# Kernel optimization log

Measured on AMD Instinct MI355X. Metric: run time of the kernel, lower is better.

## Reference

```python
import jax, jax.numpy as jnp
import numpy as np

LOC_SIZE, CID_SIZE, UID_SIZE, TIM_SIZE = 10000, 300, 1000, 48
LOC_EMB, CID_EMB, UID_EMB, TIM_EMB = 256, 64, 64, 32
HID, ENC_HID = 500, 250            # hidden_size, history_hidden_size
SEQ, TGT = 2048, 256
INPUT = LOC_EMB + TIM_EMB + CID_EMB  # 352


def setup_inputs() -> dict:
    key = jax.random.key(0)
    ks = jax.random.split(key, 32)
    n = lambda i, shape, s=0.05: (jax.random.normal(ks[i], shape, dtype=jnp.float32) * s)
    d = {}
    d["loc"] = jax.random.randint(ks[0], (SEQ, 1), 0, LOC_SIZE)
    d["tim"] = jax.random.randint(ks[1], (SEQ, 1), 0, TIM_SIZE)
    d["cid"] = jax.random.randint(ks[2], (SEQ, 1), 0, CID_SIZE)
    d["uid"] = jax.random.randint(ks[3], (1,), 0, UID_SIZE)
    d["target"] = jax.random.randint(ks[4], (TGT, 1), 0, LOC_SIZE)
    d["target_len"] = TGT
    d["time_sim_matrix"] = jax.random.uniform(ks[5], (TIM_SIZE, TIM_SIZE), dtype=jnp.float32)
    # keep distances away from 0 since the model computes 1/dist
    d["poi_distance_matrix"] = jax.random.uniform(ks[6], (LOC_SIZE, LOC_SIZE), dtype=jnp.float32, minval=0.1, maxval=2.0)
    d["poi_cid_tim"] = jax.random.uniform(ks[7], (TIM_SIZE, CID_SIZE), dtype=jnp.float32)
    # embedding tables (emb_loc/emb_cid are pretrained+frozen in the original)
    d["weight"] = n(8, (LOC_SIZE, LOC_EMB))
    d["weight_cid"] = n(9, (CID_SIZE, CID_EMB))
    d["emb_uid_w"] = n(10, (UID_SIZE, UID_EMB))
    d["emb_tim_w"] = n(11, (TIM_SIZE, TIM_EMB))
    # bidirectional encoder LSTM (hidden 250), gate order i,f,g,o like torch
    d["enc_Wih_f"] = n(12, (4 * ENC_HID, INPUT))
    d["enc_Whh_f"] = n(13, (4 * ENC_HID, ENC_HID))
    d["enc_b_f"] = jnp.zeros((4 * ENC_HID,), jnp.float32)
    d["enc_Wih_b"] = n(14, (4 * ENC_HID, INPUT))
    d["enc_Whh_b"] = n(15, (4 * ENC_HID, ENC_HID))
    d["enc_b_b"] = jnp.zeros((4 * ENC_HID,), jnp.float32)
    # decoder LSTM (hidden 500)
    d["dec_Wih"] = n(16, (4 * HID, INPUT))
    d["dec_Whh"] = n(17, (4 * HID, HID))
    d["dec_b"] = jnp.zeros((4 * HID,), jnp.float32)
    # linear layers
    d["fc_user_w"] = n(18, (HID, UID_EMB))
    d["fc_user_b"] = jnp.zeros((HID,), jnp.float32)
    d["fc_final_w"] = n(19, (LOC_SIZE, 3 * HID))
    d["fc_final_b"] = jnp.zeros((LOC_SIZE,), jnp.float32)
    d["fc_final2_w"] = n(20, (HID, 3 * HID))
    d["fc_final2_b"] = jnp.zeros((HID,), jnp.float32)
    return d


def _lstm(x, Wih, Whh, b, H):
    """Single-layer LSTM, batch=1. x: [T, D] -> hs: [T, H]."""
    h0 = jnp.zeros((H,), x.dtype)
    c0 = jnp.zeros((H,), x.dtype)

    def step(carry, xt):
        h, c = carry
        z = Wih @ xt + Whh @ h + b
        i, f, g, o = jnp.split(z, 4)
        c = jax.nn.sigmoid(f) * c + jax.nn.sigmoid(i) * jnp.tanh(g)
        h = jax.nn.sigmoid(o) * jnp.tanh(c)
        return (h, c), h

    _, hs = jax.lax.scan(step, (h0, c0), x)
    return hs


def _table_attn(history, current, table, invert=False, causal=False):
    """Vectorized replacement for the nested-loop lookup attention.
    energies[i, j] = table[current[i], history[j]] (or its reciprocal),
    upper triangle left at 0 for the self-attn variants (as in the original),
    then softmax over the full row (torch F.softmax default dim=1 on 2D)."""
    e = table[current[:, None], history[None, :]]
    if invert:
        e = 1.0 / e
    if causal:
        nn_ = e.shape[0]
        e = jnp.where(jnp.tril(jnp.ones((nn_, nn_), bool)), e, jnp.zeros((), e.dtype))
    return jax.nn.softmax(e, axis=-1)


def reference(loc, tim, cid, uid, target, target_len,
              time_sim_matrix, poi_distance_matrix, poi_cid_tim,
              weight, weight_cid, emb_uid_w, emb_tim_w,
              enc_Wih_f, enc_Whh_f, enc_b_f, enc_Wih_b, enc_Whh_b, enc_b_b,
              dec_Wih, dec_Whh, dec_b,
              fc_user_w, fc_user_b, fc_final_w, fc_final_b, fc_final2_w, fc_final2_b):
    T = int(target_len)
    loc_f, tim_f, cid_f = loc[:, 0], tim[:, 0], cid[:, 0]

    # cross attention: current window attends to history via lookup tables
    attn_cid_time = _table_attn(cid_f[:-T], tim_f[-T:], poi_cid_tim)
    attn_loc = _table_attn(loc_f[:-T], loc_f[-T:], poi_distance_matrix, invert=True)
    attn_time = _table_attn(tim_f[:-T], tim_f[-T:], time_sim_matrix)
    # self attention on the current window (lower-triangular fill)
    self_cid_time = _table_attn(cid_f[-T:], tim_f[-T:], poi_cid_tim, causal=True)
    self_loc = _table_attn(loc_f[-T:], loc_f[-T:], poi_distance_matrix, invert=True, causal=True)
    self_time = _table_attn(tim_f[-T:], tim_f[-T:], time_sim_matrix, causal=True)

    # embeddings (dropout is identity in eval)
    x = jnp.concatenate([weight[loc_f], emb_tim_w[tim_f], weight_cid[cid_f]], axis=1)  # [SEQ, INPUT]
    hist_x, tgt_x = x[:-T], x[-T:]

    # bidirectional encoder over history
    hf = _lstm(hist_x, enc_Wih_f, enc_Whh_f, enc_b_f, ENC_HID)
    hb = _lstm(hist_x[::-1], enc_Wih_b, enc_Whh_b, enc_b_b, ENC_HID)[::-1]
    hidden_history = jnp.concatenate([hf, hb], axis=1)  # [SEQ-T, 2*ENC_HID=500]

    # decoder over current window
    hidden_state = _lstm(tgt_x, dec_Wih, dec_Whh, dec_b, HID)  # [T, 500]

    target_emb = weight[target[:, 0]]  # [T, LOC_EMB]

    uid_emb = emb_uid_w[uid] @ fc_user_w.T + fc_user_b  # [1, 500]
    user_attn = jax.nn.softmax(uid_emb @ hidden_history.T, axis=-1)  # [1, hist]
    context_user = user_attn @ hidden_history  # [1, 500]

    context = (attn_loc + attn_time + attn_cid_time) @ hidden_history  # [T, 500]
    hidden_state = (self_loc + self_time + self_cid_time) @ hidden_state  # [T, 500]

    hidden_state_all = hidden_state + uid_emb  # broadcast of repeat
    out = jnp.concatenate([hidden_state_all, context,
                           jnp.broadcast_to(context_user, (T, HID))], axis=1)  # [T, 1500]
    y = out @ fc_final_w.T + fc_final_b    # [T, LOC_SIZE]
    y1 = out @ fc_final2_w.T + fc_final2_b  # [T, HID]
    score = jax.nn.log_softmax(y, axis=-1)
    return score, y1, target_emb
```

## Files before the change

kernel.cpp:

```cpp
#include <hip/hip_runtime.h>
#include <stdint.h>

#define HIST 1792
#define TGT 256
#define SEQ 2048
#define INPUT 352
#define EHID 250
#define HID 500

typedef _Float16 h2_t __attribute__((ext_vector_type(2)));

static __device__ __forceinline__ float fdot2(uint32_t a, uint32_t b, float c) {
  return __builtin_amdgcn_fdot2(__builtin_bit_cast(h2_t, a),
                                __builtin_bit_cast(h2_t, b), c, false);
}
static __device__ __forceinline__ uint32_t packh2(float lo, float hi) {
  h2_t h; h[0] = (_Float16)lo; h[1] = (_Float16)hi;
  return __builtin_bit_cast(uint32_t, h);
}
static __device__ __forceinline__ uint4 packq(const float* p) {
  uint4 r;
  r.x = packh2(p[0], p[1]); r.y = packh2(p[2], p[3]);
  r.z = packh2(p[4], p[5]); r.w = packh2(p[6], p[7]);
  return r;
}
static __device__ __forceinline__ float dotq(uint4 w, uint4 h, float acc) {
  acc = fdot2(w.x, h.x, acc); acc = fdot2(w.y, h.y, acc);
  acc = fdot2(w.z, h.z, acc); acc = fdot2(w.w, h.w, acc);
  return acc;
}
static __device__ __forceinline__ float sigf(float x) {
  x = fminf(fmaxf(x, -30.f), 30.f);
  return 1.f / (1.f + __expf(-x));
}
static __device__ __forceinline__ float tanh_f(float x) {
  x = fminf(fmaxf(x, -15.f), 15.f);
  float e = __expf(2.f * x);
  return (e - 1.f) / (e + 1.f);
}
static __device__ __forceinline__ void spin_flag(volatile int* f) {
  while (__hip_atomic_load(f, __ATOMIC_ACQUIRE, __HIP_MEMORY_SCOPE_AGENT) == 0)
    __builtin_amdgcn_s_sleep(2);
}
#define AW(dst, src) asm("v_accvgpr_write_b32 %0, %1" : "=a"(dst) : "v"(src))
#define AR(dst, src) asm("v_accvgpr_read_b32 %0, %1" : "=v"(dst) : "a"(src))
#define ARQ(dst, arr, base) do { AR(dst.x, arr[(base)+0]); AR(dst.y, arr[(base)+1]); AR(dst.z, arr[(base)+2]); AR(dst.w, arr[(base)+3]); } while(0)

__global__ void k_embed(const int* __restrict__ loc, const int* __restrict__ tim,
                        const int* __restrict__ cid, const int* __restrict__ target,
                        const float* __restrict__ weight, const float* __restrict__ emb_tim_w,
                        const float* __restrict__ weight_cid,
                        float* __restrict__ x, float* __restrict__ te) {
  int t = blockIdx.x, tid = threadIdx.x;
  if (t < SEQ) {
    int l = loc[t], tm = tim[t], cd = cid[t];
    float* xr = x + (size_t)t * INPUT;
    for (int k = tid; k < 256; k += blockDim.x) xr[k] = weight[(size_t)l * 256 + k];
    for (int k = tid; k < 32; k += blockDim.x)  xr[256 + k] = emb_tim_w[tm * 32 + k];
    for (int k = tid; k < 64; k += blockDim.x)  xr[288 + k] = weight_cid[cd * 64 + k];
  } else {
    int i = t - SEQ;
    int tg = target[i];
    for (int k = tid; k < 256; k += blockDim.x) te[(size_t)i * 256 + k] = weight[(size_t)tg * 256 + k];
  }
}

__global__ void k_gemm_t16(const float* __restrict__ A, int lda,
                           const float* __restrict__ W, const float* __restrict__ bias,
                           float* __restrict__ C, int ldc,
                           int M, int N, int K, int revA) {
  __shared__ uint32_t AsP[8][65];
  __shared__ uint32_t WsP[8][65];
  const int bn = blockIdx.x * 64, bm = blockIdx.y * 64;
  const int tid = threadIdx.x;
  const int tx = tid & 15, ty = tid >> 4;
  float acc[4][4] = {};
  for (int k0 = 0; k0 < K; k0 += 16) {
    for (int i = tid; i < 512; i += 256) {
      int m = i & 63, kk = i >> 6;
      int gm = bm + m, gk = k0 + 2 * kk;
      float v0 = 0.f, v1 = 0.f;
      if (gm < M) {
        int am = revA ? (M - 1 - gm) : gm;
        if (gk < K)     v0 = A[(size_t)am * lda + gk];
        if (gk + 1 < K) v1 = A[(size_t)am * lda + gk + 1];
      }
      AsP[kk][m] = packh2(v0, v1);
    }
    for (int i = tid; i < 512; i += 256) {
      int n = i & 63, kk = i >> 6;
      int gn = bn + n, gk = k0 + 2 * kk;
      float v0 = 0.f, v1 = 0.f;
      if (gn < N) {
        if (gk < K)     v0 = W[(size_t)gn * K + gk];
        if (gk + 1 < K) v1 = W[(size_t)gn * K + gk + 1];
      }
      WsP[kk][n] = packh2(v0, v1);
    }
    __syncthreads();
#pragma unroll
    for (int kk = 0; kk < 8; kk++) {
      uint32_t a0 = AsP[kk][ty * 4 + 0], a1 = AsP[kk][ty * 4 + 1], a2 = AsP[kk][ty * 4 + 2], a3 = AsP[kk][ty * 4 + 3];
      uint32_t b0 = WsP[kk][tx * 4 + 0], b1 = WsP[kk][tx * 4 + 1], b2 = WsP[kk][tx * 4 + 2], b3 = WsP[kk][tx * 4 + 3];
      acc[0][0] = fdot2(a0, b0, acc[0][0]); acc[0][1] = fdot2(a0, b1, acc[0][1]);
      acc[0][2] = fdot2(a0, b2, acc[0][2]); acc[0][3] = fdot2(a0, b3, acc[0][3]);
      acc[1][0] = fdot2(a1, b0, acc[1][0]); acc[1][1] = fdot2(a1, b1, acc[1][1]);
      acc[1][2] = fdot2(a1, b2, acc[1][2]); acc[1][3] = fdot2(a1, b3, acc[1][3]);
      acc[2][0] = fdot2(a2, b0, acc[2][0]); acc[2][1] = fdot2(a2, b1, acc[2][1]);
      acc[2][2] = fdot2(a2, b2, acc[2][2]); acc[2][3] = fdot2(a2, b3, acc[2][3]);
      acc[3][0] = fdot2(a3, b0, acc[3][0]); acc[3][1] = fdot2(a3, b1, acc[3][1]);
      acc[3][2] = fdot2(a3, b2, acc[3][2]); acc[3][3] = fdot2(a3, b3, acc[3][3]);
    }
    __syncthreads();
  }
  for (int i = 0; i < 4; i++) {
    int gm = bm + ty * 4 + i; if (gm >= M) continue;
    for (int j = 0; j < 4; j++) {
      int gn = bn + tx * 4 + j; if (gn >= N) continue;
      C[(size_t)gm * ldc + gn] = acc[i][j] + (bias ? bias[gn] : 0.f);
    }
  }
}

__global__ void k_gemm_nn16(const float* __restrict__ A, int lda,
                            const float* __restrict__ B, int ldb,
                            const float* __restrict__ addvec,
                            float* __restrict__ C, int ldc,
                            int M, int N, int K) {
  __shared__ uint32_t AsP[8][65];
  __shared__ uint32_t BsP[8][65];
  const int bn = blockIdx.x * 64, bm = blockIdx.y * 64;
  const int tid = threadIdx.x;
  const int tx = tid & 15, ty = tid >> 4;
  float acc[4][4] = {};
  for (int k0 = 0; k0 < K; k0 += 16) {
    for (int i = tid; i < 512; i += 256) {
      int m = i & 63, kk = i >> 6;
      int gm = bm + m, gk = k0 + 2 * kk;
      float v0 = 0.f, v1 = 0.f;
      if (gm < M) {
        if (gk < K)     v0 = A[(size_t)gm * lda + gk];
        if (gk + 1 < K) v1 = A[(size_t)gm * lda + gk + 1];
      }
      AsP[kk][m] = packh2(v0, v1);
    }
    for (int i = tid; i < 512; i += 256) {
      int n = i & 63, kk = i >> 6;
      int gn = bn + n, gk = k0 + 2 * kk;
      float v0 = 0.f, v1 = 0.f;
      if (gn < N) {
        if (gk < K)     v0 = B[(size_t)gk * ldb + gn];
        if (gk + 1 < K) v1 = B[(size_t)(gk + 1) * ldb + gn];
      }
      BsP[kk][n] = packh2(v0, v1);
    }
    __syncthreads();
#pragma unroll
    for (int kk = 0; kk < 8; kk++) {
      uint32_t a0 = AsP[kk][ty * 4 + 0], a1 = AsP[kk][ty * 4 + 1], a2 = AsP[kk][ty * 4 + 2], a3 = AsP[kk][ty * 4 + 3];
      uint32_t b0 = BsP[kk][tx * 4 + 0], b1 = BsP[kk][tx * 4 + 1], b2 = BsP[kk][tx * 4 + 2], b3 = BsP[kk][tx * 4 + 3];
      acc[0][0] = fdot2(a0, b0, acc[0][0]); acc[0][1] = fdot2(a0, b1, acc[0][1]);
      acc[0][2] = fdot2(a0, b2, acc[0][2]); acc[0][3] = fdot2(a0, b3, acc[0][3]);
      acc[1][0] = fdot2(a1, b0, acc[1][0]); acc[1][1] = fdot2(a1, b1, acc[1][1]);
      acc[1][2] = fdot2(a1, b2, acc[1][2]); acc[1][3] = fdot2(a1, b3, acc[1][3]);
      acc[2][0] = fdot2(a2, b0, acc[2][0]); acc[2][1] = fdot2(a2, b1, acc[2][1]);
      acc[2][2] = fdot2(a2, b2, acc[2][2]); acc[2][3] = fdot2(a2, b3, acc[2][3]);
      acc[3][0] = fdot2(a3, b0, acc[3][0]); acc[3][1] = fdot2(a3, b1, acc[3][1]);
      acc[3][2] = fdot2(a3, b2, acc[3][2]); acc[3][3] = fdot2(a3, b3, acc[3][3]);
    }
    __syncthreads();
  }
  for (int i = 0; i < 4; i++) {
    int gm = bm + ty * 4 + i; if (gm >= M) continue;
    for (int j = 0; j < 4; j++) {
      int gn = bn + tx * 4 + j; if (gn >= N) continue;
      C[(size_t)gm * ldc + gn] = acc[i][j] + (addvec ? addvec[gn] : 0.f);
    }
  }
}

#define WQL 12
#define WBYTES (WQL * 512 * 16)
__launch_bounds__(512)
__global__ void k_lstm(const float* __restrict__ A_f, const float* __restrict__ A_b,
                       const float* __restrict__ A_d,
                       const float* __restrict__ Whh_f, const float* __restrict__ Whh_b,
                       const float* __restrict__ Whh_d,
                       float* __restrict__ hh, float* __restrict__ hdec,
                       float* zpub, uint32_t* hpub, int* flag_z, int* flag_h,
                       const int* __restrict__ loc, const int* __restrict__ tim,
                       const int* __restrict__ cid,
                       const float* __restrict__ ts, const float* __restrict__ pd,
                       const float* __restrict__ pct,
                       float* __restrict__ S1, float* __restrict__ S2,
                       const int* __restrict__ uid, const float* __restrict__ emb_uid_w,
                       const float* __restrict__ fc_user_w, const float* __restrict__ fc_user_b,
                       float* __restrict__ uid_emb) {
  const int b = blockIdx.x;
  const int tid = threadIdx.x;
  __shared__ __align__(16) unsigned char smem[WBYTES + 2048 + 4096];
  uint4* wl = (uint4*)smem;
  uint4* hbuf = (uint4*)(smem + WBYTES);
  float* zbuf = (float*)(smem + WBYTES + 2048);

  if (b < 6 && tid < 128) hbuf[tid] = make_uint4(0, 0, 0, 0);

  if (b < 2) {
    const float* A = (b == 0) ? A_f : A_b;
    const float* Whh = (b == 0) ? Whh_f : Whh_b;
    const bool act = tid < 500;
    uint4 wv0[10], wv1[10];
    uint32_t wa[128];
    if (act) {
      const float* wr0 = Whh + (size_t)tid * EHID;
      const float* wr1 = Whh + (size_t)(tid + 500) * EHID;
#pragma unroll
      for (int q = 0; q < 6; q++) {
        float t0[8], t1[8];
#pragma unroll
        for (int cc = 0; cc < 8; cc++) {
          int col = 208 + 8 * q + cc;
          t0[cc] = (col < EHID) ? wr0[col] : 0.f;
          t1[cc] = (col < EHID) ? wr1[col] : 0.f;
        }
        wl[(q * 2 + 0) * 512 + tid] = packq(t0);
        wl[(q * 2 + 1) * 512 + tid] = packq(t1);
      }
#pragma unroll
      for (int k = 0; k < 16; k++) {
        uint4 p0 = packq(wr0 + 8 * (10 + k));
        uint4 p1 = packq(wr1 + 8 * (10 + k));
        AW(wa[k * 4 + 0], p0.x); AW(wa[k * 4 + 1], p0.y);
        AW(wa[k * 4 + 2], p0.z); AW(wa[k * 4 + 3], p0.w);
        AW(wa[64 + k * 4 + 0], p1.x); AW(wa[64 + k * 4 + 1], p1.y);
        AW(wa[64 + k * 4 + 2], p1.z); AW(wa[64 + k * 4 + 3], p1.w);
      }
#pragma unroll
      for (int q = 0; q < 10; q++) { wv0[q] = packq(wr0 + 8 * q); wv1[q] = packq(wr1 + 8 * q); }
    }
    float c = 0.f;
    float aA = act ? A[tid] : 0.f;
    float aB = act ? A[500 + tid] : 0.f;
    __syncthreads();
    for (int t = 0; t < HIST; t++) {
      const uint4* hb = hbuf + (t & 1) * 32;
      if (act) {
        float z0 = aA, z1 = aB, y0 = 0.f, y1 = 0.f;
        int tn = (t + 1 < HIST) ? t + 1 : t;
        aA = A[tn * 1000 + tid];
        aB = A[tn * 1000 + 500 + tid];
#pragma unroll
        for (int q = 0; q < 10; q++) {
          uint4 hq = hb[q];
          z0 = dotq(wv0[q], hq, z0);
          z1 = dotq(wv1[q], hq, z1);
        }
#pragma unroll
        for (int k = 0; k < 16; k++) {
          uint4 hq = hb[10 + k];
          uint4 u0, u1;
          ARQ(u0, wa, k * 4);
          ARQ(u1, wa, 64 + k * 4);
          y0 = dotq(u0, hq, y0);
          y1 = dotq(u1, hq, y1);
        }
#pragma unroll
        for (int q = 0; q < 6; q++) {
          uint4 hq = hb[26 + q];
          z0 = dotq(wl[(q * 2 + 0) * 512 + tid], hq, z0);
          z1 = dotq(wl[(q * 2 + 1) * 512 + tid], hq, z1);
        }
        zbuf[tid] = z0 + y0;
        zbuf[500 + tid] = z1 + y1;
      }
      __syncthreads();
      float hval = 0.f;
      if (tid < EHID) {
        float zi = zbuf[tid], zf = zbuf[250 + tid], zg = zbuf[500 + tid], zo = zbuf[750 + tid];
        c = sigf(zf) * c + sigf(zi) * tanh_f(zg);
        hval = sigf(zo) * tanh_f(c);
        if (b == 0) hh[(size_t)t * HID + tid] = hval;
        else        hh[(size_t)(HIST - 1 - t) * HID + EHID + tid] = hval;
      }
      float hother = __shfl_xor(hval, 1);
      uint32_t* hw = (uint32_t*)(hbuf + ((t + 1) & 1) * 32);
      if (tid < EHID && !(tid & 1)) hw[tid >> 1] = packh2(hval, hother);
      __syncthreads();
    }
  } else if (b < 6) {
    const int gi = b - 2;
    const int j = tid;
    const bool act = (j < 500);
    uint4 wv[20];
    uint32_t wa[128];
    if (act) {
      const float* wr = Whh_d + (size_t)(gi * 500 + j) * HID;
#pragma unroll
      for (int q = 0; q < 12; q++) {
        float tmp[8];
#pragma unroll
        for (int cc = 0; cc < 8; cc++) {
          int col = 416 + 8 * q + cc;
          tmp[cc] = (col < HID) ? wr[col] : 0.f;
        }
        wl[q * 512 + tid] = packq(tmp);
      }
#pragma unroll
      for (int k = 0; k < 32; k++) {
        uint4 pq = packq(wr + 8 * (20 + k));
        AW(wa[k * 4 + 0], pq.x); AW(wa[k * 4 + 1], pq.y);
        AW(wa[k * 4 + 2], pq.z); AW(wa[k * 4 + 3], pq.w);
      }
#pragma unroll
      for (int q = 0; q < 20; q++) wv[q] = packq(wr + 8 * q);
    }
    float c = 0.f;
    float aD = act ? A_d[gi * 500 + j] : 0.f;
    __syncthreads();
    for (int t = 0; t < TGT; t++) {
      const uint4* hb = hbuf + (t & 1) * 64;
      float z = 0.f;
      if (act) {
        float z0 = aD, z1 = 0.f, z2 = 0.f, z3 = 0.f;
        int tn = (t + 1 < TGT) ? t + 1 : t;
        aD = A_d[tn * 2000 + gi * 500 + j];
#pragma unroll
        for (int q = 0; q < 20; q += 2) {
          z0 = dotq(wv[q], hb[q], z0);
          z1 = dotq(wv[q + 1], hb[q + 1], z1);
        }
#pragma unroll
        for (int k = 0; k < 32; k += 2) {
          uint4 u0, u1;
          ARQ(u0, wa, k * 4);
          ARQ(u1, wa, (k + 1) * 4);
          z2 = dotq(u0, hb[20 + k], z2);
          z3 = dotq(u1, hb[21 + k], z3);
        }
#pragma unroll
        for (int q = 0; q < 12; q += 2) {
          z0 = dotq(wl[q * 512 + tid], hb[52 + q], z0);
          z1 = dotq(wl[(q + 1) * 512 + tid], hb[53 + q], z1);
        }
        z = (z0 + z1) + (z2 + z3);
      }
      if (gi < 3) {
        if (act) zpub[gi * 512 + j] = z;
        __threadfence();
        __syncthreads();
        if (tid == 0) {
          __hip_atomic_store(&flag_z[t * 3 + gi], 1, __ATOMIC_RELEASE, __HIP_MEMORY_SCOPE_AGENT);
          spin_flag(&flag_h[t]);
        }
        __syncthreads();
        uint32_t* hw = (uint32_t*)(hbuf + ((t + 1) & 1) * 64);
        if (tid < 250)
          hw[tid] = __hip_atomic_load(&hpub[tid], __ATOMIC_RELAXED, __HIP_MEMORY_SCOPE_AGENT);
        __syncthreads();
      } else {
        if (tid == 0) {
          spin_flag(&flag_z[t * 3 + 0]);
          spin_flag(&flag_z[t * 3 + 1]);
          spin_flag(&flag_z[t * 3 + 2]);
        }
        __syncthreads();
        float hval = 0.f;
        if (act) {
          float zi = __hip_atomic_load(&zpub[0 * 512 + j], __ATOMIC_RELAXED, __HIP_MEMORY_SCOPE_AGENT);
          float zf = __hip_atomic_load(&zpub[1 * 512 + j], __ATOMIC_RELAXED, __HIP_MEMORY_SCOPE_AGENT);
          float zg = __hip_atomic_load(&zpub[2 * 512 + j], __ATOMIC_RELAXED, __HIP_MEMORY_SCOPE_AGENT);
          c = sigf(zf) * c + sigf(zi) * tanh_f(zg);
          hval = sigf(z) * tanh_f(c);
          hdec[(size_t)t * HID + j] = hval;
        }
        float hother = __shfl_xor(hval, 1);
        uint32_t* hw = (uint32_t*)(hbuf + ((t + 1) & 1) * 64);
        if (act && !(j & 1)) {
          uint32_t p = packh2(hval, hother);
          hw[j >> 1] = p;
          __hip_atomic_store(&hpub[j >> 1], p, __ATOMIC_RELAXED, __HIP_MEMORY_SCOPE_AGENT);
        }
        __threadfence();
        __syncthreads();
        if (tid == 0)
          __hip_atomic_store(&flag_h[t], 1, __ATOMIC_RELEASE, __HIP_MEMORY_SCOPE_AGENT);
      }
    }
  } else if (b < 262) {
    const int i = b - 6;
    float* e = (float*)smem;
    float* red = ((float*)smem) + HIST;
    const int loc_i = loc[HIST + i], tim_i = tim[HIST + i];
    for (int tab = 0; tab < 3; tab++) {
      for (int jj = tid; jj < HIST; jj += 512) {
        float v;
        if (tab == 0)      v = 1.f / pd[(size_t)loc_i * 10000 + loc[jj]];
        else if (tab == 1) v = ts[tim_i * 48 + tim[jj]];
        else               v = pct[tim_i * 300 + cid[jj]];
        e[jj] = v;
      }
      __syncthreads();
      float mx = -1e30f;
      for (int jj = tid; jj < HIST; jj += 512) mx = fmaxf(mx, e[jj]);
      red[tid] = mx; __syncthreads();
      for (int s = 256; s > 0; s >>= 1) { if (tid < s) red[tid] = fmaxf(red[tid], red[tid + s]); __syncthreads(); }
      mx = red[0]; __syncthreads();
      float sm = 0.f;
      for (int jj = tid; jj < HIST; jj += 512) sm += __expf(e[jj] - mx);
      red[tid] = sm; __syncthreads();
      for (int s = 256; s > 0; s >>= 1) { if (tid < s) red[tid] += red[tid + s]; __syncthreads(); }
      float inv = 1.f / red[0]; __syncthreads();
      for (int jj = tid; jj < HIST; jj += 512) {
        float p = __expf(e[jj] - mx) * inv;
        if (tab == 0) S1[(size_t)i * HIST + jj] = p; else S1[(size_t)i * HIST + jj] += p;
      }
      __syncthreads();
    }
    int lj = 0, tj = 0, cj = 0;
    if (tid < TGT) { lj = loc[HIST + tid]; tj = tim[HIST + tid]; cj = cid[HIST + tid]; }
    for (int tab = 0; tab < 3; tab++) {
      float v = 0.f;
      if (tid < TGT) {
        if (tab == 0)      v = 1.f / pd[(size_t)loc_i * 10000 + lj];
        else if (tab == 1) v = ts[tim_i * 48 + tj];
        else               v = pct[tim_i * 300 + cj];
        if (tid > i) v = 0.f;
        red[tid] = v;
      }
      __syncthreads();
      for (int s = 128; s > 0; s >>= 1) { if (tid < s) red[tid] = fmaxf(red[tid], red[tid + s]); __syncthreads(); }
      float mx = red[0]; __syncthreads();
      float ex = (tid < TGT) ? __expf(v - mx) : 0.f;
      if (tid < TGT) red[tid] = ex;
      __syncthreads();
      for (int s = 128; s > 0; s >>= 1) { if (tid < s) red[tid] += red[tid + s]; __syncthreads(); }
      float p = ex / red[0]; __syncthreads();
      if (tid < TGT) {
        if (tab == 0) S2[(size_t)i * TGT + tid] = p; else S2[(size_t)i * TGT + tid] += p;
      }
      __syncthreads();
    }
  } else {
    float* u = (float*)smem;
    if (tid < 64) u[tid] = emb_uid_w[(size_t)uid[0] * 64 + tid];
    __syncthreads();
    if (tid < HID) {
      float a = fc_user_b[tid];
      for (int k = 0; k < 64; k++) a += u[k] * fc_user_w[tid * 64 + k];
      uid_emb[tid] = a;
    }
  }
}

__global__ void k_user(const float* __restrict__ uid_emb, const float* __restrict__ hh,
                       float* __restrict__ out) {
  const int tid = threadIdx.x;
  __shared__ float s[HIST];
  __shared__ float red[1024];
  __shared__ __align__(16) float ue[HID];
  if (tid < HID) ue[tid] = uid_emb[tid];
  __syncthreads();
  for (int t = tid; t < HIST; t += 1024) {
    const float4* hr = (const float4*)(hh + (size_t)t * HID);
    const float4* uv = (const float4*)ue;
    float a = 0.f;
#pragma unroll 5
    for (int k = 0; k < 125; k++) {
      float4 h4 = hr[k], u4 = uv[k];
      a += h4.x * u4.x + h4.y * u4.y + h4.z * u4.z + h4.w * u4.w;
    }
    s[t] = a;
  }
  __syncthreads();
  float mx = -1e30f;
  for (int t = tid; t < HIST; t += 1024) mx = fmaxf(mx, s[t]);
  red[tid] = mx; __syncthreads();
  for (int st = 512; st > 0; st >>= 1) { if (tid < st) red[tid] = fmaxf(red[tid], red[tid + st]); __syncthreads(); }
  mx = red[0]; __syncthreads();
  float sm = 0.f;
  for (int t = tid; t < HIST; t += 1024) sm += __expf(s[t] - mx);
  red[tid] = sm; __syncthreads();
  for (int st = 512; st > 0; st >>= 1) { if (tid < st) red[tid] += red[tid + st]; __syncthreads(); }
  float inv = 1.f / red[0]; __syncthreads();
  for (int t = tid; t < HIST; t += 1024) s[t] = __expf(s[t] - mx) * inv;
  __syncthreads();
  if (tid < HID) {
    float a0 = 0.f, a1 = 0.f, a2 = 0.f, a3 = 0.f;
    for (int t = 0; t < HIST; t += 4) {
      a0 += s[t]     * hh[(size_t)t * HID + tid];
      a1 += s[t + 1] * hh[(size_t)(t + 1) * HID + tid];
      a2 += s[t + 2] * hh[(size_t)(t + 2) * HID + tid];
      a3 += s[t + 3] * hh[(size_t)(t + 3) * HID + tid];
    }
    float a = (a0 + a1) + (a2 + a3);
    for (int i = 0; i < TGT; i++) out[(size_t)i * 1500 + 1000 + tid] = a;
  }
}

__global__ void k_logsoftmax(float* __restrict__ y) {
  const int i = blockIdx.x;
  const int tid = threadIdx.x;
  float* r = y + (size_t)i * 10000;
  __shared__ float red[1024];
  float mx = -1e30f;
  for (int j = tid; j < 10000; j += 1024) mx = fmaxf(mx, r[j]);
  red[tid] = mx; __syncthreads();
  for (int s = 512; s > 0; s >>= 1) { if (tid < s) red[tid] = fmaxf(red[tid], red[tid + s]); __syncthreads(); }
  mx = red[0]; __syncthreads();
  float sm = 0.f;
  for (int j = tid; j < 10000; j += 1024) sm += __expf(r[j] - mx);
  red[tid] = sm; __syncthreads();
  for (int s = 512; s > 0; s >>= 1) { if (tid < s) red[tid] += red[tid + s]; __syncthreads(); }
  float lse = mx + __logf(red[0]);
  __syncthreads();
  for (int j = tid; j < 10000; j += 1024) r[j] = r[j] - lse;
}

extern "C" void kernel_launch(void* const* d_in, const int* in_sizes, int n_in,
                              void* d_out, int out_size, void* d_ws, size_t ws_size,
                              hipStream_t stream) {
  (void)in_sizes; (void)n_in; (void)out_size; (void)ws_size;
  const int* loc = (const int*)d_in[0];
  const int* tim = (const int*)d_in[1];
  const int* cid = (const int*)d_in[2];
  const int* uid = (const int*)d_in[3];
  const int* target = (const int*)d_in[4];
  const float* ts = (const float*)d_in[6];
  const float* pd = (const float*)d_in[7];
  const float* pct = (const float*)d_in[8];
  const float* weight = (const float*)d_in[9];
  const float* weight_cid = (const float*)d_in[10];
  const float* emb_uid_w = (const float*)d_in[11];
  const float* emb_tim_w = (const float*)d_in[12];
  const float* enc_Wih_f = (const float*)d_in[13];
  const float* enc_Whh_f = (const float*)d_in[14];
  const float* enc_b_f = (const float*)d_in[15];
  const float* enc_Wih_b = (const float*)d_in[16];
  const float* enc_Whh_b = (const float*)d_in[17];
  const float* enc_b_b = (const float*)d_in[18];
  const float* dec_Wih = (const float*)d_in[19];
  const float* dec_Whh = (const float*)d_in[20];
  const float* dec_b = (const float*)d_in[21];
  const float* fc_user_w = (const float*)d_in[22];
  const float* fc_user_b = (const float*)d_in[23];
  const float* fc_final_w = (const float*)d_in[24];
  const float* fc_final_b = (const float*)d_in[25];
  const float* fc_final2_w = (const float*)d_in[26];
  const float* fc_final2_b = (const float*)d_in[27];

  float* score = (float*)d_out;
  float* y1 = score + (size_t)TGT * 10000;
  float* te = y1 + (size_t)TGT * HID;

  float* ws = (float*)d_ws;
  float* x = ws;
  float* A_f = x + (size_t)SEQ * INPUT;
  float* A_b = A_f + (size_t)HIST * 1000;
  float* A_d = A_b + (size_t)HIST * 1000;
  float* hh = A_d + (size_t)TGT * 2000;
  float* hdec = hh + (size_t)HIST * HID;
  float* S1 = hdec + (size_t)TGT * HID;
  float* S2 = S1 + (size_t)TGT * HIST;
  float* outb = S2 + (size_t)TGT * TGT;
  float* uid_emb = outb + (size_t)TGT * 1500;
  float* zpub = uid_emb + 512;
  uint32_t* hpub = (uint32_t*)(zpub + 3 * 512);
  int* flag_z = (int*)(hpub + 256);
  int* flag_h = flag_z + 3 * TGT;

  k_embed<<<dim3(SEQ + TGT), dim3(128), 0, stream>>>(loc, tim, cid, target, weight, emb_tim_w, weight_cid, x, te);

  k_gemm_t16<<<dim3(16, 28), dim3(256), 0, stream>>>(x, INPUT, enc_Wih_f, enc_b_f, A_f, 1000, HIST, 1000, INPUT, 0);
  k_gemm_t16<<<dim3(16, 28), dim3(256), 0, stream>>>(x, INPUT, enc_Wih_b, enc_b_b, A_b, 1000, HIST, 1000, INPUT, 1);
  k_gemm_t16<<<dim3(32, 4), dim3(256), 0, stream>>>(x + (size_t)HIST * INPUT, INPUT, dec_Wih, dec_b, A_d, 2000, TGT, 2000, INPUT, 0);

  hipMemsetAsync(flag_z, 0, 4 * TGT * sizeof(int), stream);

  k_lstm<<<dim3(263), dim3(512), 0, stream>>>(A_f, A_b, A_d, enc_Whh_f, enc_Whh_b, dec_Whh,
                                              hh, hdec, zpub, hpub, flag_z, flag_h,
                                              loc, tim, cid, ts, pd, pct, S1, S2,
                                              uid, emb_uid_w, fc_user_w, fc_user_b, uid_emb);

  k_user<<<dim3(1), dim3(1024), 0, stream>>>(uid_emb, hh, outb);
  k_gemm_nn16<<<dim3(8, 4), dim3(256), 0, stream>>>(S2, TGT, hdec, HID, uid_emb, outb, 1500, TGT, HID, TGT);
  k_gemm_nn16<<<dim3(8, 4), dim3(256), 0, stream>>>(S1, HIST, hh, HID, nullptr, outb + 500, 1500, TGT, HID, HIST);

  k_gemm_t16<<<dim3(157, 4), dim3(256), 0, stream>>>(outb, 1500, fc_final_w, fc_final_b, score, 10000, TGT, 10000, 1500, 0);
  k_gemm_t16<<<dim3(8, 4), dim3(256), 0, stream>>>(outb, 1500, fc_final2_w, fc_final2_b, y1, 500, TGT, 500, 1500, 0);

  k_logsoftmax<<<dim3(TGT), dim3(1024), 0, stream>>>(score);
}
```

Measured before the change: 5.322 ms.

## Fuse input-projection GEMMs into LSTM kernel with chunk counters; fold user context into bias

Moves the encoder and decoder input-projection GEMMs into the persistent LSTM launch as extra blocks. Each block publishes completion through per-chunk atomic counters, and the recurrent blocks spin on those counters before consuming each 64-step chunk. This lets the recurrence start before all projections finish and removes separate launches. It also folds the constant context_user columns of the final linear layers into a precomputed bias, so the final GEMMs run with K=1000 instead of 1500. The risk is deadlock if the recurrent blocks are resident while the GEMM blocks cannot get scheduled, plus extra spin overhead.

```diff
diff --git a/kernel.cpp b/kernel.cpp
--- a/kernel.cpp
+++ b/kernel.cpp
@@ -40,6 +40,10 @@
 }
 static __device__ __forceinline__ void spin_flag(volatile int* f) {
   while (__hip_atomic_load(f, __ATOMIC_ACQUIRE, __HIP_MEMORY_SCOPE_AGENT) == 0)
+    __builtin_amdgcn_s_sleep(2);
+}
+static __device__ __forceinline__ void spin_cnt(volatile int* f, int target) {
+  while (__hip_atomic_load(f, __ATOMIC_ACQUIRE, __HIP_MEMORY_SCOPE_AGENT) < target)
     __builtin_amdgcn_s_sleep(2);
 }
 #define AW(dst, src) asm("v_accvgpr_write_b32 %0, %1" : "=a"(dst) : "v"(src))
@@ -66,7 +70,8 @@
 }
 
 __global__ void k_gemm_t16(const float* __restrict__ A, int lda,
-                           const float* __restrict__ W, const float* __restrict__ bias,
+                           const float* __restrict__ W, int ldw,
+                           const float* __restrict__ bias,
                            float* __restrict__ C, int ldc,
                            int M, int N, int K, int revA) {
   __shared__ uint32_t AsP[8][65];
@@ -92,8 +97,8 @@
       int gn = bn + n, gk = k0 + 2 * kk;
       float v0 = 0.f, v1 = 0.f;
       if (gn < N) {
-        if (gk < K)     v0 = W[(size_t)gn * K + gk];
-        if (gk + 1 < K) v1 = W[(size_t)gn * K + gk + 1];
+        if (gk < K)     v0 = W[(size_t)gn * ldw + gk];
+        if (gk + 1 < K) v1 = W[(size_t)gn * ldw + gk + 1];
       }
       WsP[kk][n] = packh2(v0, v1);
     }
@@ -179,15 +184,77 @@
   }
 }
 
+static __device__ void gemm_tile_fused(const float* __restrict__ A, int lda,
+                                       const float* __restrict__ W,
+                                       const float* __restrict__ bias,
+                                       float* __restrict__ C, int ldc,
+                                       int M, int N, int bm, int bn, int revA,
+                                       int tid, uint32_t* AsP, uint32_t* WsP) {
+  const int tx = tid & 15, ty = (tid & 255) >> 4;
+  float acc[4][4] = {};
+  for (int k0 = 0; k0 < INPUT; k0 += 16) {
+    {
+      int m = tid & 63, kk = tid >> 6;
+      int gm = bm + m, gk = k0 + 2 * kk;
+      float v0 = 0.f, v1 = 0.f;
+      if (gm < M) {
+        int am = revA ? (M - 1 - gm) : gm;
+        if (gk < INPUT)     v0 = A[(size_t)am * lda + gk];
+        if (gk + 1 < INPUT) v1 = A[(size_t)am * lda + gk + 1];
+      }
+      AsP[kk * 65 + m] = packh2(v0, v1);
+      int gn = bn + m;
+      float w0 = 0.f, w1 = 0.f;
+      if (gn < N) {
+        if (gk < INPUT)     w0 = W[(size_t)gn * INPUT + gk];
+        if (gk + 1 < INPUT) w1 = W[(size_t)gn * INPUT + gk + 1];
+      }
+      WsP[kk * 65 + m] = packh2(w0, w1);
+    }
+    __syncthreads();
+    if (tid < 256) {
+#pragma unroll
+      for (int kk = 0; kk < 8; kk++) {
+        uint32_t a0 = AsP[kk * 65 + ty * 4 + 0], a1 = AsP[kk * 65 + ty * 4 + 1];
+        uint32_t a2 = AsP[kk * 65 + ty * 4 + 2], a3 = AsP[kk * 65 + ty * 4 + 3];
+        uint32_t b0 = WsP[kk * 65 + tx * 4 + 0], b1 = WsP[kk * 65 + tx * 4 + 1];
+        uint32_t b2 = WsP[kk * 65 + tx * 4 + 2], b3 = WsP[kk * 65 + tx * 4 + 3];
+        acc[0][0] = fdot2(a0, b0, acc[0][0]); acc[0][1] = fdot2(a0, b1, acc[0][1]);
+        acc[0][2] = fdot2(a0, b2, acc[0][2]); acc[0][3] = fdot2(a0, b3, acc[0][3]);
+        acc[1][0] = fdot2(a1, b0, acc[1][0]); acc[1][1] = fdot2(a1, b1, acc[1][1]);
+        acc[1][2] = fdot2(a1, b2, acc[1][2]); acc[1][3] = fdot2(a1, b3, acc[1][3]);
+        acc[2][0] = fdot2(a2, b0, acc[2][0]); acc[2][1] = fdot2(a2, b1, acc[2][1]);
+        acc[2][2] = fdot2(a2, b2, acc[2][2]); acc[2][3] = fdot2(a2, b3, acc[2][3]);
+        acc[3][0] = fdot2(a3, b0, acc[3][0]); acc[3][1] = fdot2(a3, b1, acc[3][1]);
+        acc[3][2] = fdot2(a3, b2, acc[3][2]); acc[3][3] = fdot2(a3, b3, acc[3][3]);
+      }
+    }
+    __syncthreads();
+  }
+  if (tid < 256) {
+    for (int i = 0; i < 4; i++) {
+      int gm = bm + ty * 4 + i; if (gm >= M) continue;
+      for (int j = 0; j < 4; j++) {
+        int gn = bn + tx * 4 + j; if (gn >= N) continue;
+        C[(size_t)gm * ldc + gn] = acc[i][j] + bias[gn];
+      }
+    }
+  }
+}
+
 #define WQL 12
 #define WBYTES (WQL * 512 * 16)
 __launch_bounds__(512)
-__global__ void k_lstm(const float* __restrict__ A_f, const float* __restrict__ A_b,
-                       const float* __restrict__ A_d,
+__global__ void k_lstm(const float* __restrict__ x,
+                       float* __restrict__ A_f, float* __restrict__ A_b,
+                       float* __restrict__ A_d,
+                       const float* __restrict__ Wih_f, const float* __restrict__ b_f,
+                       const float* __restrict__ Wih_b, const float* __restrict__ b_b,
+                       const float* __restrict__ Wih_d, const float* __restrict__ b_d,
                        const float* __restrict__ Whh_f, const float* __restrict__ Whh_b,
                        const float* __restrict__ Whh_d,
                        float* __restrict__ hh, float* __restrict__ hdec,
-                       float* zpub, uint32_t* hpub, int* flag_z, int* flag_h,
+                       float* zpub, uint32_t* hpub, int* flag_z, int* flag_h, int* cnt,
                        const int* __restrict__ loc, const int* __restrict__ tim,
                        const int* __restrict__ cid,
                        const float* __restrict__ ts, const float* __restrict__ pd,
@@ -206,8 +273,9 @@
   if (b < 6 && tid < 128) hbuf[tid] = make_uint4(0, 0, 0, 0);
 
   if (b < 2) {
-    const float* A = (b == 0) ? A_f : A_b;
+    float* A = (b == 0) ? A_f : A_b;
     const float* Whh = (b == 0) ? Whh_f : Whh_b;
+    int* mycnt = cnt + b * 32;
     const bool act = tid < 500;
     uint4 wv0[10], wv1[10];
     uint32_t wa[128];
@@ -238,15 +306,21 @@
 #pragma unroll
       for (int q = 0; q < 10; q++) { wv0[q] = packq(wr0 + 8 * q); wv1[q] = packq(wr1 + 8 * q); }
     }
+    if (tid == 0) spin_cnt(&mycnt[0], 16);
+    __syncthreads();
     float c = 0.f;
     float aA = act ? A[tid] : 0.f;
     float aB = act ? A[500 + tid] : 0.f;
     __syncthreads();
     for (int t = 0; t < HIST; t++) {
       const uint4* hb = hbuf + (t & 1) * 32;
+      int tn = (t + 1 < HIST) ? t + 1 : t;
+      if ((tn & 63) == 0 && tn > t) {
+        if (tid == 0) spin_cnt(&mycnt[tn >> 6], 16);
+        __syncthreads();
+      }
       if (act) {
         float z0 = aA, z1 = aB, y0 = 0.f, y1 = 0.f;
-        int tn = (t + 1 < HIST) ? t + 1 : t;
         aA = A[tn * 1000 + tid];
         aB = A[tn * 1000 + 500 + tid];
 #pragma unroll
@@ -291,6 +365,7 @@
     const int gi = b - 2;
     const int j = tid;
     const bool act = (j < 500);
+    int* dcnt = cnt + 64;
     uint4 wv[20];
     uint32_t wa[128];
     if (act) {
@@ -314,15 +389,21 @@
 #pragma unroll
       for (int q = 0; q < 20; q++) wv[q] = packq(wr + 8 * q);
     }
+    if (tid == 0) spin_cnt(&dcnt[0], 32);
+    __syncthreads();
     float c = 0.f;
     float aD = act ? A_d[gi * 500 + j] : 0.f;
     __syncthreads();
     for (int t = 0; t < TGT; t++) {
       const uint4* hb = hbuf + (t & 1) * 64;
+      int tn = (t + 1 < TGT) ? t + 1 : t;
+      if ((tn & 63) == 0 && tn > t) {
+        if (tid == 0) spin_cnt(&dcnt[tn >> 6], 32);
+        __syncthreads();
+      }
       float z = 0.f;
       if (act) {
         float z0 = aD, z1 = 0.f, z2 = 0.f, z3 = 0.f;
-        int tn = (t + 1 < TGT) ? t + 1 : t;
         aD = A_d[tn * 2000 + gi * 500 + j];
 #pragma unroll
         for (int q = 0; q < 20; q += 2) {
@@ -386,8 +467,48 @@
           __hip_atomic_store(&flag_h[t], 1, __ATOMIC_RELEASE, __HIP_MEMORY_SCOPE_AGENT);
       }
     }
-  } else if (b < 262) {
-    const int i = b - 6;
+  } else if (b == 6) {
+    float* u = (float*)smem;
+    if (tid < 64) u[tid] = emb_uid_w[(size_t)uid[0] * 64 + tid];
+    __syncthreads();
+    if (tid < HID) {
+      float a = fc_user_b[tid];
+      for (int k = 0; k < 64; k++) a += u[k] * fc_user_w[tid * 64 + k];
+      uid_emb[tid] = a;
+    }
+  } else if (b < 903) {
+    const int g = b - 7;
+    const int chunk = g >> 5, w = g & 31;
+    uint32_t* AsP = (uint32_t*)smem;
+    uint32_t* WsP = AsP + 8 * 65;
+    if (w < 16) {
+      gemm_tile_fused(x, INPUT, Wih_f, b_f, A_f, 1000, HIST, 1000,
+                      chunk * 64, w * 64, 0, tid, AsP, WsP);
+      __threadfence();
+      __syncthreads();
+      if (tid == 0)
+        __hip_atomic_fetch_add(&cnt[chunk], 1, __ATOMIC_RELEASE, __HIP_MEMORY_SCOPE_AGENT);
+    } else {
+      gemm_tile_fused(x, INPUT, Wih_b, b_b, A_b, 1000, HIST, 1000,
+                      chunk * 64, (w - 16) * 64, 1, tid, AsP, WsP);
+      __threadfence();
+      __syncthreads();
+      if (tid == 0)
+        __hip_atomic_fetch_add(&cnt[32 + chunk], 1, __ATOMIC_RELEASE, __HIP_MEMORY_SCOPE_AGENT);
+    }
+  } else if (b < 1031) {
+    const int g = b - 903;
+    const int mt = g >> 5, nt = g & 31;
+    uint32_t* AsP = (uint32_t*)smem;
+    uint32_t* WsP = AsP + 8 * 65;
+    gemm_tile_fused(x + (size_t)HIST * INPUT, INPUT, Wih_d, b_d, A_d, 2000, TGT, 2000,
+                    mt * 64, nt * 64, 0, tid, AsP, WsP);
+    __threadfence();
+    __syncthreads();
+    if (tid == 0)
+      __hip_atomic_fetch_add(&cnt[64 + mt], 1, __ATOMIC_RELEASE, __HIP_MEMORY_SCOPE_AGENT);
+  } else {
+    const int i = b - 1031;
     float* e = (float*)smem;
     float* red = ((float*)smem) + HIST;
     const int loc_i = loc[HIST + i], tim_i = tim[HIST + i];
@@ -440,20 +561,11 @@
       }
       __syncthreads();
     }
-  } else {
-    float* u = (float*)smem;
-    if (tid < 64) u[tid] = emb_uid_w[(size_t)uid[0] * 64 + tid];
-    __syncthreads();
-    if (tid < HID) {
-      float a = fc_user_b[tid];
-      for (int k = 0; k < 64; k++) a += u[k] * fc_user_w[tid * 64 + k];
-      uid_emb[tid] = a;
-    }
   }
 }
 
 __global__ void k_user(const float* __restrict__ uid_emb, const float* __restrict__ hh,
-                       float* __restrict__ out) {
+                       float* __restrict__ cu) {
   const int tid = threadIdx.x;
   __shared__ float s[HIST];
   __shared__ float red[1024];
@@ -492,8 +604,39 @@
       a2 += s[t + 2] * hh[(size_t)(t + 2) * HID + tid];
       a3 += s[t + 3] * hh[(size_t)(t + 3) * HID + tid];
     }
-    float a = (a0 + a1) + (a2 + a3);
-    for (int i = 0; i < TGT; i++) out[(size_t)i * 1500 + 1000 + tid] = a;
+    cu[tid] = (a0 + a1) + (a2 + a3);
+  }
+}
+
+__global__ void k_cubias(const float* __restrict__ cu,
+                         const float* __restrict__ Wf, const float* __restrict__ bf,
+                         const float* __restrict__ W2, const float* __restrict__ b2,
+                         float* __restrict__ fb, float* __restrict__ fb2) {
+  __shared__ __align__(16) float cus[HID];
+  const int tid = threadIdx.x;
+  if (tid < 250) { cus[tid] = cu[tid]; cus[250 + tid] = cu[250 + tid]; }
+  __syncthreads();
+  int n = blockIdx.x * 256 + tid;
+  const float4* cv = (const float4*)cus;
+  if (n < 10000) {
+    const float4* w = (const float4*)(Wf + (size_t)n * 1500 + 1000);
+    float a = bf[n];
+#pragma unroll 5
+    for (int k = 0; k < 125; k++) {
+      float4 wv = w[k], uv = cv[k];
+      a += wv.x * uv.x + wv.y * uv.y + wv.z * uv.z + wv.w * uv.w;
+    }
+    fb[n] = a;
+  } else if (n < 10500) {
+    int m = n - 10000;
+    const float4* w = (const float4*)(W2 + (size_t)m * 1500 + 1000);
+    float a = b2[m];
+#pragma unroll 5
+    for (int k = 0; k < 125; k++) {
+      float4 wv = w[k], uv = cv[k];
+      a += wv.x * uv.x + wv.y * uv.y + wv.z * uv.z + wv.w * uv.w;
+    }
+    fb2[m] = a;
   }
 }
 
@@ -562,31 +705,37 @@
   float* S1 = hdec + (size_t)TGT * HID;
   float* S2 = S1 + (size_t)TGT * HIST;
   float* outb = S2 + (size_t)TGT * TGT;
-  float* uid_emb = outb + (size_t)TGT * 1500;
+  float* cu = outb + (size_t)TGT * 1000;
+  float* fb = cu + 512;
+  float* fb2 = fb + 10016;
+  float* uid_emb = fb2 + 512;
   float* zpub = uid_emb + 512;
   uint32_t* hpub = (uint32_t*)(zpub + 3 * 512);
   int* flag_z = (int*)(hpub + 256);
   int* flag_h = flag_z + 3 * TGT;
+  int* cnt = flag_h + TGT;
+  const int n_flags = 4 * TGT + 96;
 
   k_embed<<<dim3(SEQ + TGT), dim3(128), 0, stream>>>(loc, tim, cid, target, weight, emb_tim_w, weight_cid, x, te);
 
-  k_gemm_t16<<<dim3(16, 28), dim3(256), 0, stream>>>(x, INPUT, enc_Wih_f, enc_b_f, A_f, 1000, HIST, 1000, INPUT, 0);
-  k_gemm_t16<<<dim3(16, 28), dim3(256), 0, stream>>>(x, INPUT, enc_Wih_b, enc_b_b, A_b, 1000, HIST, 1000, INPUT, 1);
-  k_gemm_t16<<<dim3(32, 4), dim3(256), 0, stream>>>(x + (size_t)HIST * INPUT, INPUT, dec_Wih, dec_b, A_d, 2000, TGT, 2000, INPUT, 0);
-
-  hipMemsetAsync(flag_z, 0, 4 * TGT * sizeof(int), stream);
-
-  k_lstm<<<dim3(263), dim3(512), 0, stream>>>(A_f, A_b, A_d, enc_Whh_f, enc_Whh_b, dec_Whh,
-                                              hh, hdec, zpub, hpub, flag_z, flag_h,
-                                              loc, tim, cid, ts, pd, pct, S1, S2,
-                                              uid, emb_uid_w, fc_user_w, fc_user_b, uid_emb);
-
-  k_user<<<dim3(1), dim3(1024), 0, stream>>>(uid_emb, hh, outb);
-  k_gemm_nn16<<<dim3(8, 4), dim3(256), 0, stream>>>(S2, TGT, hdec, HID, uid_emb, outb, 1500, TGT, HID, TGT);
-  k_gemm_nn16<<<dim3(8, 4), dim3(256), 0, stream>>>(S1, HIST, hh, HID, nullptr, outb + 500, 1500, TGT, HID, HIST);
-
-  k_gemm_t16<<<dim3(157, 4), dim3(256), 0, stream>>>(outb, 1500, fc_final_w, fc_final_b, score, 10000, TGT, 10000, 1500, 0);
-  k_gemm_t16<<<dim3(8, 4), dim3(256), 0, stream>>>(outb, 1500, fc_final2_w, fc_final2_b, y1, 500, TGT, 500, 1500, 0);
+  hipMemsetAsync(flag_z, 0, n_flags * sizeof(int), stream);
+
+  k_lstm<<<dim3(1287), dim3(512), 0, stream>>>(x, A_f, A_b, A_d,
+                                               enc_Wih_f, enc_b_f, enc_Wih_b, enc_b_b,
+                                               dec_Wih, dec_b,
+                                               enc_Whh_f, enc_Whh_b, dec_Whh,
+                                               hh, hdec, zpub, hpub, flag_z, flag_h, cnt,
+                                               loc, tim, cid, ts, pd, pct, S1, S2,
+                                               uid, emb_uid_w, fc_user_w, fc_user_b, uid_emb);
+
+  k_user<<<dim3(1), dim3(1024), 0, stream>>>(uid_emb, hh, cu);
+  k_cubias<<<dim3(42), dim3(256), 0, stream>>>(cu, fc_final_w, fc_final_b,
+                                               fc_final2_w, fc_final2_b, fb, fb2);
+  k_gemm_nn16<<<dim3(8, 4), dim3(256), 0, stream>>>(S2, TGT, hdec, HID, uid_emb, outb, 1000, TGT, HID, TGT);
+  k_gemm_nn16<<<dim3(8, 4), dim3(256), 0, stream>>>(S1, HIST, hh, HID, nullptr, outb + 500, 1000, TGT, HID, HIST);
+
+  k_gemm_t16<<<dim3(157, 4), dim3(256), 0, stream>>>(outb, 1000, fc_final_w, 1500, fb, score, 10000, TGT, 10000, 1000, 0);
+  k_gemm_t16<<<dim3(8, 4), dim3(256), 0, stream>>>(outb, 1000, fc_final2_w, 1500, fb2, y1, 500, TGT, 500, 1000, 0);
 
   k_logsoftmax<<<dim3(TGT), dim3(1024), 0, stream>>>(score);
 }
```

Measured after the change: 4.835 ms. -9.1%, faster.
